# Performance work log

Hardware: AMD Instinct MI355X
Metric: run time of the kernel (lower is better)

Reference implementation:

```python
import jax, jax.numpy as jnp
import numpy as np

B, T, I, H = 256, 256, 256, 1024
STATE_DIM = 2
TAU = 0.05
MHU = 1.5


def setup_inputs() -> dict:
    key = jax.random.key(0)
    ks = jax.random.split(key, 6)
    s_in, s_h = 1.0 / np.sqrt(I), 1.0 / np.sqrt(H)
    return {
        "rnn_input": jax.random.normal(ks[0], (B, T, I), jnp.float32),
        "h0": jax.random.normal(ks[1], (1, B, H), jnp.float32),
        "c0": jax.random.normal(ks[2], (1, B, H), jnp.float32),
        "Wx": jax.random.normal(ks[3], (I, 4 * H), jnp.float32) * s_in,
        "Wh": jax.random.normal(ks[4], (H, 4 * H), jnp.float32) * s_h,
        "b": jax.random.normal(ks[5], (4 * H,), jnp.float32) * 0.01,
    }


def reference(rnn_input, h0, c0, Wx, Wh, b):
    # A: hard-coded 2x2 drift matrix applied to h[:, :STATE_DIM] for t>0
    A = jnp.array([[MHU, -MHU], [1.0 / MHU, 0.0]], dtype=rnn_input.dtype)
    hdim = Wh.shape[0]

    def step(carry, xs):
        h, c = carry                      # [B,H], [B,H]
        u_t, not_first = xs               # [B,I], scalar bool
        x_prev = h[:, :STATE_DIM]         # [B,2]
        x_next = jnp.where(not_first, x_prev + TAU * (x_prev @ A), x_prev)
        h = h.at[:, :STATE_DIM].set(x_next)
        gates = u_t @ Wx + h @ Wh + b     # [B,4H], gate order i,f,g,o
        i, f, g, o = jnp.split(gates, 4, axis=-1)
        i, f, o = jax.nn.sigmoid(i), jax.nn.sigmoid(f), jax.nn.sigmoid(o)
        g = jnp.tanh(g)
        c_next = f * c + i * g
        h_next = o * jnp.tanh(c_next)
        return (h_next, c_next), h_next

    u_seq = jnp.swapaxes(rnn_input, 0, 1)          # [T,B,I]
    not_first = jnp.arange(u_seq.shape[0]) > 0     # [T]
    (hN, cN), ys = jax.lax.scan(step, (h0[0], c0[0]), (u_seq, not_first))
    outputs = jnp.swapaxes(ys, 0, 1)               # [B,T,H] (batch_first)
    return outputs, hN[None], cN[None]
```

## Files before the change

### kernel.cpp

```cpp
#include <hip/hip_runtime.h>
#include <hip/hip_bf16.h>

#define Bdim 256
#define Tdim 256
#define Idim 256
#define Hdim 1024
#define KDIM 1280
#define NP   4096

typedef __attribute__((ext_vector_type(8)))  short short8;
typedef __attribute__((ext_vector_type(4)))  short short4v;
typedef __attribute__((ext_vector_type(16))) float f32x16;
typedef unsigned long long u64;

__device__ __forceinline__ short f2bf(float f) {
  unsigned u = __builtin_bit_cast(unsigned, f);
  unsigned r = (u + 0x7FFFu + ((u >> 16) & 1u)) >> 16;
  return (short)r;
}
__device__ __forceinline__ float bf2f(short s) {
  unsigned u = ((unsigned)(unsigned short)s) << 16;
  return __builtin_bit_cast(float, u);
}

__global__ void setup_wt_kernel(const float* __restrict__ Wx,
                                const float* __restrict__ Wh,
                                short* __restrict__ Wt) {
  __shared__ float tile[64 * 65];
  const int nb = blockIdx.x, kb = blockIdx.y;
  const int tid = threadIdx.x;
#pragma unroll
  for (int i = 0; i < 16; ++i) {
    int idx = i * 256 + tid;
    int kr = idx >> 6, nc = idx & 63;
    int kglob = kb * 64 + kr;
    int np = nb * 64 + nc;
    int col = ((np & 3) << 10) | (np >> 2);
    float v = (kglob < Idim) ? Wx[(size_t)kglob * NP + col]
                             : Wh[(size_t)(kglob - Idim) * NP + col];
    tile[kr * 65 + nc] = v;
  }
  __syncthreads();
#pragma unroll
  for (int i = 0; i < 16; ++i) {
    int idx = i * 256 + tid;
    int nr = idx >> 6, kc = idx & 63;
    Wt[(size_t)(nb * 64 + nr) * KDIM + kb * 64 + kc] = f2bf(tile[kc * 65 + nr]);
  }
}

__global__ void setup_state_kernel(const float* __restrict__ h0,
                                   const float* __restrict__ c0,
                                   const float* __restrict__ b,
                                   short* __restrict__ Uh0,
                                   float* __restrict__ c_state,
                                   float* __restrict__ bp,
                                   unsigned* __restrict__ bar) {
  if (blockIdx.x == 1041) {
    if (threadIdx.x < 256) bar[threadIdx.x] = 0u;
    return;
  }
  int idx = blockIdx.x * 256 + threadIdx.x;
  if (blockIdx.x < 1024) {
    Uh0[idx] = f2bf(h0[idx]);
    c_state[idx] = c0[idx];
  } else if (blockIdx.x < 1040) {
    int j = idx - 1024 * 256;
    if (j < NP) bp[j] = b[((j & 3) << 10) | (j >> 2)];
  }
}

__global__ __launch_bounds__(512) __attribute__((amdgpu_waves_per_eu(2, 2)))
void lstm_persistent(
    const float* __restrict__ xin,
    const short* __restrict__ Wt,
    const float* __restrict__ bp,
    short* __restrict__ Uh0,
    short* __restrict__ Uh1,
    float* __restrict__ out,
    float* __restrict__ c_state,
    float* __restrict__ hN,
    unsigned* __restrict__ bar) {
  __shared__ __align__(16) short As[32 * KDIM];
  __shared__ __align__(16) float Gred[2][32][132];

  const int tid  = threadIdx.x;
  const int lane = tid & 63;
  const int wave = tid >> 6;
  const int ntl  = wave & 3;
  const int kh   = wave >> 2;
  const int m    = blockIdx.x & 7;
  const int ng   = blockIdx.x >> 3;
  const int bm0  = m * 32;
  const int n0   = ng * 128 + ntl * 32;

  short8 Wreg[40];
  {
    const short* wr = Wt + (size_t)(n0 + (lane & 31)) * KDIM + kh * 640 + ((lane >> 5) << 3);
#pragma unroll
    for (int ks = 0; ks < 40; ++ks) Wreg[ks] = *(const short8*)(wr + ks * 16);
  }
#pragma unroll
  for (int ks = 0; ks < 40; ++ks) asm volatile("" : "+v"(Wreg[ks]));

  const int arow  = lane & 31;
  const int rbase = arow * 2560 + kh * 1280 + ((lane >> 5) << 4);
  const int rxor  = (arow & 15) << 4;

  const int row0 = tid >> 7;
  const int c8   = (tid & 127) << 3;

  const int erow = tid >> 4;
  const int ep   = tid & 15;
  const float4 bb0 = ((const float4*)bp)[ng * 32 + 2 * ep];
  const float4 bb1 = ((const float4*)bp)[ng * 32 + 2 * ep + 1];

  unsigned* flags = bar + m * 32;

  for (int t = 0; t < Tdim; ++t) {
    const short* UhR = (t & 1) ? Uh1 : Uh0;
    short* UhW = (t & 1) ? Uh0 : Uh1;

#pragma unroll
    for (int i = 0; i < 2; ++i) {
      int unit = i * 512 + tid;
      int row = unit >> 5, cx = (unit & 31) << 3;
      const float* p = xin + (size_t)(bm0 + row) * (Tdim * Idim) + (size_t)t * Idim + cx;
      float4 a = *(const float4*)p, b4 = *(const float4*)(p + 4);
      short8 v;
      v[0] = f2bf(a.x);  v[1] = f2bf(a.y);  v[2] = f2bf(a.z);  v[3] = f2bf(a.w);
      v[4] = f2bf(b4.x); v[5] = f2bf(b4.y); v[6] = f2bf(b4.z); v[7] = f2bf(b4.w);
      *(short8*)((char*)As + (((row * 2560) + (cx << 1)) ^ ((row & 15) << 4))) = v;
    }
    {
      const short* hbase = UhR + (size_t)(bm0 + row0) * Hdim + c8;
#pragma unroll
      for (int i = 0; i < 8; ++i) {
        const short* hp = hbase + (size_t)(4 * i) * Hdim;
        u64 lo = __hip_atomic_load((const u64*)hp, __ATOMIC_RELAXED,
                                   __HIP_MEMORY_SCOPE_AGENT);
        u64 hi = __hip_atomic_load((const u64*)(hp + 4), __ATOMIC_RELAXED,
                                   __HIP_MEMORY_SCOPE_AGENT);
        short4v vlo = __builtin_bit_cast(short4v, lo);
        short4v vhi = __builtin_bit_cast(short4v, hi);
        if (t > 0 && c8 == 0) {
          float x0 = bf2f(vlo[0]), x1 = bf2f(vlo[1]);
          vlo[0] = f2bf(x0 + 0.05f * (1.5f * x0 + (1.0f / 1.5f) * x1));
          vlo[1] = f2bf(x1 - 0.05f * 1.5f * x0);
        }
        int row = row0 + 4 * i;
        char* dst = (char*)As + (((row * 2560) + ((256 + c8) << 1)) ^ ((row & 15) << 4));
        *(short4v*)dst = vlo;
        *(short4v*)(dst + 8) = vhi;
      }
    }
    __syncthreads();

    f32x16 acc;
#pragma unroll
    for (int i = 0; i < 16; ++i) acc[i] = 0.f;
#pragma unroll
    for (int ks = 0; ks < 40; ++ks) {
      short8 a = *(const short8*)((char*)As + ((rbase + ks * 32) ^ rxor));
      acc = __builtin_amdgcn_mfma_f32_32x32x16_bf16(a, Wreg[ks], acc, 0, 0, 0);
    }

    {
      const int col = lane & 31, half = lane >> 5;
#pragma unroll
      for (int r = 0; r < 16; ++r) {
        int rl = (r & 3) + 8 * (r >> 2) + 4 * half;
        Gred[kh][rl][ntl * 32 + col] = acc[r];
      }
    }
    __syncthreads();

    {
      float4 a0 = *(const float4*)&Gred[0][erow][8 * ep];
      float4 a1 = *(const float4*)&Gred[0][erow][8 * ep + 4];
      float4 d0 = *(const float4*)&Gred[1][erow][8 * ep];
      float4 d1 = *(const float4*)&Gred[1][erow][8 * ep + 4];
      float gx0 = a0.x + d0.x + bb0.x, gy0 = a0.y + d0.y + bb0.y;
      float gz0 = a0.z + d0.z + bb0.z, gw0 = a0.w + d0.w + bb0.w;
      float gx1 = a1.x + d1.x + bb1.x, gy1 = a1.y + d1.y + bb1.y;
      float gz1 = a1.z + d1.z + bb1.z, gw1 = a1.w + d1.w + bb1.w;
      float iv0 = 1.0f / (1.0f + __expf(-gx0));
      float fv0 = 1.0f / (1.0f + __expf(-gy0));
      float gg0 = 2.0f / (1.0f + __expf(-2.0f * gz0)) - 1.0f;
      float ov0 = 1.0f / (1.0f + __expf(-gw0));
      float iv1 = 1.0f / (1.0f + __expf(-gx1));
      float fv1 = 1.0f / (1.0f + __expf(-gy1));
      float gg1 = 2.0f / (1.0f + __expf(-2.0f * gz1)) - 1.0f;
      float ov1 = 1.0f / (1.0f + __expf(-gw1));
      int bm = bm0 + erow;
      int hu0 = ng * 32 + 2 * ep;
      size_t cidx = (size_t)bm * Hdim + hu0;
      float2 cold = *(const float2*)&c_state[cidx];
      float cn0 = fv0 * cold.x + iv0 * gg0;
      float cn1 = fv1 * cold.y + iv1 * gg1;
      *(float2*)&c_state[cidx] = make_float2(cn0, cn1);
      float hv0 = ov0 * (2.0f / (1.0f + __expf(-2.0f * cn0)) - 1.0f);
      float hv1 = ov1 * (2.0f / (1.0f + __expf(-2.0f * cn1)) - 1.0f);
      *(float2*)&out[(size_t)bm * (Tdim * Hdim) + (size_t)t * Hdim + hu0] =
          make_float2(hv0, hv1);
      unsigned hpk = (unsigned)(unsigned short)f2bf(hv0) |
                     ((unsigned)(unsigned short)f2bf(hv1) << 16);
      __hip_atomic_store((unsigned*)&UhW[cidx], hpk, __ATOMIC_RELAXED,
                         __HIP_MEMORY_SCOPE_AGENT);
      if (t == Tdim - 1) *(float2*)&hN[cidx] = make_float2(hv0, hv1);
    }

    if (t < Tdim - 1) {
      asm volatile("s_waitcnt vmcnt(0)" ::: "memory");
      __syncthreads();
      if (wave == 0) {
        if (lane == 0)
          __hip_atomic_store(&flags[ng], (unsigned)(t + 1), __ATOMIC_RELAXED,
                             __HIP_MEMORY_SCOPE_AGENT);
        const unsigned tgt = (unsigned)(t + 1);
        for (;;) {
          unsigned v = __hip_atomic_load(&flags[lane & 31], __ATOMIC_RELAXED,
                                         __HIP_MEMORY_SCOPE_AGENT);
          if (__all((int)(v >= tgt))) break;
          __builtin_amdgcn_s_sleep(2);
        }
      }
      __syncthreads();
    }
  }
}

extern "C" void kernel_launch(void* const* d_in, const int* in_sizes, int n_in,
                              void* d_out, int out_size, void* d_ws, size_t ws_size,
                              hipStream_t stream) {
  const float* xin = (const float*)d_in[0];
  const float* h0  = (const float*)d_in[1];
  const float* c0  = (const float*)d_in[2];
  const float* Wx  = (const float*)d_in[3];
  const float* Wh  = (const float*)d_in[4];
  const float* b   = (const float*)d_in[5];
  float* out = (float*)d_out;

  char* ws = (char*)d_ws;
  short* Wt  = (short*)ws;
  short* Uh0 = (short*)(ws + 10485760);
  short* Uh1 = (short*)(ws + 10485760 + 524288);
  float* bp  = (float*)(ws + 10485760 + 1048576);
  unsigned* bar = (unsigned*)(ws + 10485760 + 1048576 + 16384);

  float* hN      = out + (size_t)Bdim * Tdim * Hdim;
  float* c_state = hN + (size_t)Bdim * Hdim;

  setup_wt_kernel<<<dim3(64, 20), 256, 0, stream>>>(Wx, Wh, Wt);
  setup_state_kernel<<<1042, 256, 0, stream>>>(h0, c0, b, Uh0, c_state, bp, bar);

  void* args[] = {(void*)&xin, (void*)&Wt, (void*)&bp, (void*)&Uh0, (void*)&Uh1,
                  (void*)&out, (void*)&c_state, (void*)&hN, (void*)&bar};
  hipLaunchCooperativeKernel((const void*)lstm_persistent, dim3(256), dim3(512),
                             args, 0, stream);
}
```

Before: 2.220 ms.

## Precompute next-step input projection during barrier wait and keep cell state in registers

Splits the shared A tile into separate input and hidden buffers. The input-projection MFMAs for step t+1 now run before the inter-block barrier wait, taking them off the critical path that follows the barrier. Input rows are prefetched two steps ahead into registers, and the cell state stays in registers, written back only once at the end. The spin-wait sleep is also shortened. The cost is more register pressure (extra prefetch registers alongside 40 weight fragments) and a changed K-split mapping of weights per wave.

```diff
diff --git a/kernel.cpp b/kernel.cpp
--- a/kernel.cpp
+++ b/kernel.cpp
@@ -81,7 +81,8 @@
     float* __restrict__ c_state,
     float* __restrict__ hN,
     unsigned* __restrict__ bar) {
-  __shared__ __align__(16) short As[32 * KDIM];
+  __shared__ __align__(16) short Asx[32 * 256];
+  __shared__ __align__(16) short Ash[32 * 1024];
   __shared__ __align__(16) float Gred[2][32][132];
 
   const int tid  = threadIdx.x;
@@ -93,19 +94,29 @@
   const int ng   = blockIdx.x >> 3;
   const int bm0  = m * 32;
   const int n0   = ng * 128 + ntl * 32;
+  const int lrow = lane & 31;
+  const int koff = (lane >> 5) << 3;
 
   short8 Wreg[40];
   {
-    const short* wr = Wt + (size_t)(n0 + (lane & 31)) * KDIM + kh * 640 + ((lane >> 5) << 3);
-#pragma unroll
-    for (int ks = 0; ks < 40; ++ks) Wreg[ks] = *(const short8*)(wr + ks * 16);
+    const short* wr = Wt + (size_t)(n0 + lrow) * KDIM + koff;
+#pragma unroll
+    for (int j = 0; j < 8; ++j)  Wreg[j]     = *(const short8*)(wr + kh * 128 + j * 16);
+#pragma unroll
+    for (int j = 0; j < 32; ++j) Wreg[8 + j] = *(const short8*)(wr + 256 + kh * 512 + j * 16);
   }
 #pragma unroll
   for (int ks = 0; ks < 40; ++ks) asm volatile("" : "+v"(Wreg[ks]));
 
-  const int arow  = lane & 31;
-  const int rbase = arow * 2560 + kh * 1280 + ((lane >> 5) << 4);
-  const int rxor  = (arow & 15) << 4;
+  const int axor = (lrow & 15) << 4;
+  const int xfb  = lrow * 512  + kh * 256  + ((lane >> 5) << 4);
+  const int hfb  = lrow * 2048 + kh * 1024 + ((lane >> 5) << 4);
+
+  const int xr = tid >> 4;
+  const int xc = (tid & 15) << 4;
+  const float* xp_base = xin + (size_t)(bm0 + xr) * (Tdim * Idim) + xc;
+  const int xw0 = xr * 512 + xc * 2;
+  const int xwx = (xr & 15) << 4;
 
   const int row0 = tid >> 7;
   const int c8   = (tid & 127) << 3;
@@ -114,29 +125,66 @@
   const int ep   = tid & 15;
   const float4 bb0 = ((const float4*)bp)[ng * 32 + 2 * ep];
   const float4 bb1 = ((const float4*)bp)[ng * 32 + 2 * ep + 1];
+  const int hu0 = ng * 32 + 2 * ep;
+  const size_t cidx = (size_t)(bm0 + erow) * Hdim + hu0;
+  float2 cReg = *(const float2*)&c_state[cidx];
+  float2 hLast = make_float2(0.f, 0.f);
 
   unsigned* flags = bar + m * 32;
+
+  {
+    const float* p = xp_base;
+    float4 a0 = *(const float4*)p,     a1 = *(const float4*)(p + 4);
+    float4 a2 = *(const float4*)(p + 8), a3 = *(const float4*)(p + 12);
+    short8 v0, v1;
+    v0[0]=f2bf(a0.x); v0[1]=f2bf(a0.y); v0[2]=f2bf(a0.z); v0[3]=f2bf(a0.w);
+    v0[4]=f2bf(a1.x); v0[5]=f2bf(a1.y); v0[6]=f2bf(a1.z); v0[7]=f2bf(a1.w);
+    v1[0]=f2bf(a2.x); v1[1]=f2bf(a2.y); v1[2]=f2bf(a2.z); v1[3]=f2bf(a2.w);
+    v1[4]=f2bf(a3.x); v1[5]=f2bf(a3.y); v1[6]=f2bf(a3.z); v1[7]=f2bf(a3.w);
+    *(short8*)((char*)Asx + (xw0 ^ xwx)) = v0;
+    *(short8*)((char*)Asx + ((xw0 + 16) ^ xwx)) = v1;
+  }
+  float4 rX0, rX1, rX2, rX3;
+  {
+    const float* p = xp_base + Idim;
+    rX0 = *(const float4*)p;      rX1 = *(const float4*)(p + 4);
+    rX2 = *(const float4*)(p + 8); rX3 = *(const float4*)(p + 12);
+  }
+  __syncthreads();
+  f32x16 acc;
+#pragma unroll
+  for (int i = 0; i < 16; ++i) acc[i] = 0.f;
+#pragma unroll
+  for (int ks = 0; ks < 8; ++ks) {
+    short8 a = *(const short8*)((char*)Asx + ((xfb + ks * 32) ^ axor));
+    acc = __builtin_amdgcn_mfma_f32_32x32x16_bf16(a, Wreg[ks], acc, 0, 0, 0);
+  }
+  __syncthreads();
 
   for (int t = 0; t < Tdim; ++t) {
     const short* UhR = (t & 1) ? Uh1 : Uh0;
     short* UhW = (t & 1) ? Uh0 : Uh1;
 
-#pragma unroll
-    for (int i = 0; i < 2; ++i) {
-      int unit = i * 512 + tid;
-      int row = unit >> 5, cx = (unit & 31) << 3;
-      const float* p = xin + (size_t)(bm0 + row) * (Tdim * Idim) + (size_t)t * Idim + cx;
-      float4 a = *(const float4*)p, b4 = *(const float4*)(p + 4);
-      short8 v;
-      v[0] = f2bf(a.x);  v[1] = f2bf(a.y);  v[2] = f2bf(a.z);  v[3] = f2bf(a.w);
-      v[4] = f2bf(b4.x); v[5] = f2bf(b4.y); v[6] = f2bf(b4.z); v[7] = f2bf(b4.w);
-      *(short8*)((char*)As + (((row * 2560) + (cx << 1)) ^ ((row & 15) << 4))) = v;
-    }
+    if (t < Tdim - 1) {
+      short8 v0, v1;
+      v0[0]=f2bf(rX0.x); v0[1]=f2bf(rX0.y); v0[2]=f2bf(rX0.z); v0[3]=f2bf(rX0.w);
+      v0[4]=f2bf(rX1.x); v0[5]=f2bf(rX1.y); v0[6]=f2bf(rX1.z); v0[7]=f2bf(rX1.w);
+      v1[0]=f2bf(rX2.x); v1[1]=f2bf(rX2.y); v1[2]=f2bf(rX2.z); v1[3]=f2bf(rX2.w);
+      v1[4]=f2bf(rX3.x); v1[5]=f2bf(rX3.y); v1[6]=f2bf(rX3.z); v1[7]=f2bf(rX3.w);
+      *(short8*)((char*)Asx + (xw0 ^ xwx)) = v0;
+      *(short8*)((char*)Asx + ((xw0 + 16) ^ xwx)) = v1;
+    }
+    if (t < Tdim - 2) {
+      const float* p = xp_base + (size_t)(t + 2) * Idim;
+      rX0 = *(const float4*)p;       rX1 = *(const float4*)(p + 4);
+      rX2 = *(const float4*)(p + 8); rX3 = *(const float4*)(p + 12);
+    }
+
     {
-      const short* hbase = UhR + (size_t)(bm0 + row0) * Hdim + c8;
+      const short* hb = UhR + (size_t)(bm0 + row0) * Hdim + c8;
 #pragma unroll
       for (int i = 0; i < 8; ++i) {
-        const short* hp = hbase + (size_t)(4 * i) * Hdim;
+        const short* hp = hb + (size_t)(4 * i) * Hdim;
         u64 lo = __hip_atomic_load((const u64*)hp, __ATOMIC_RELAXED,
                                    __HIP_MEMORY_SCOPE_AGENT);
         u64 hi = __hip_atomic_load((const u64*)(hp + 4), __ATOMIC_RELAXED,
@@ -149,20 +197,17 @@
           vlo[1] = f2bf(x1 - 0.05f * 1.5f * x0);
         }
         int row = row0 + 4 * i;
-        char* dst = (char*)As + (((row * 2560) + ((256 + c8) << 1)) ^ ((row & 15) << 4));
+        char* dst = (char*)Ash + (((row * 2048) + (c8 << 1)) ^ ((row & 15) << 4));
         *(short4v*)dst = vlo;
         *(short4v*)(dst + 8) = vhi;
       }
     }
     __syncthreads();
 
-    f32x16 acc;
-#pragma unroll
-    for (int i = 0; i < 16; ++i) acc[i] = 0.f;
-#pragma unroll
-    for (int ks = 0; ks < 40; ++ks) {
-      short8 a = *(const short8*)((char*)As + ((rbase + ks * 32) ^ rxor));
-      acc = __builtin_amdgcn_mfma_f32_32x32x16_bf16(a, Wreg[ks], acc, 0, 0, 0);
+#pragma unroll
+    for (int ks = 0; ks < 32; ++ks) {
+      short8 a = *(const short8*)((char*)Ash + ((hfb + ks * 32) ^ axor));
+      acc = __builtin_amdgcn_mfma_f32_32x32x16_bf16(a, Wreg[8 + ks], acc, 0, 0, 0);
     }
 
     {
@@ -192,25 +237,28 @@
       float fv1 = 1.0f / (1.0f + __expf(-gy1));
       float gg1 = 2.0f / (1.0f + __expf(-2.0f * gz1)) - 1.0f;
       float ov1 = 1.0f / (1.0f + __expf(-gw1));
-      int bm = bm0 + erow;
-      int hu0 = ng * 32 + 2 * ep;
-      size_t cidx = (size_t)bm * Hdim + hu0;
-      float2 cold = *(const float2*)&c_state[cidx];
-      float cn0 = fv0 * cold.x + iv0 * gg0;
-      float cn1 = fv1 * cold.y + iv1 * gg1;
-      *(float2*)&c_state[cidx] = make_float2(cn0, cn1);
+      float cn0 = fv0 * cReg.x + iv0 * gg0;
+      float cn1 = fv1 * cReg.y + iv1 * gg1;
+      cReg = make_float2(cn0, cn1);
       float hv0 = ov0 * (2.0f / (1.0f + __expf(-2.0f * cn0)) - 1.0f);
       float hv1 = ov1 * (2.0f / (1.0f + __expf(-2.0f * cn1)) - 1.0f);
-      *(float2*)&out[(size_t)bm * (Tdim * Hdim) + (size_t)t * Hdim + hu0] =
-          make_float2(hv0, hv1);
       unsigned hpk = (unsigned)(unsigned short)f2bf(hv0) |
                      ((unsigned)(unsigned short)f2bf(hv1) << 16);
       __hip_atomic_store((unsigned*)&UhW[cidx], hpk, __ATOMIC_RELAXED,
                          __HIP_MEMORY_SCOPE_AGENT);
-      if (t == Tdim - 1) *(float2*)&hN[cidx] = make_float2(hv0, hv1);
+      *(float2*)&out[(size_t)(bm0 + erow) * (Tdim * Hdim) + (size_t)t * Hdim + hu0] =
+          make_float2(hv0, hv1);
+      hLast = make_float2(hv0, hv1);
     }
 
     if (t < Tdim - 1) {
+#pragma unroll
+      for (int i = 0; i < 16; ++i) acc[i] = 0.f;
+#pragma unroll
+      for (int ks = 0; ks < 8; ++ks) {
+        short8 a = *(const short8*)((char*)Asx + ((xfb + ks * 32) ^ axor));
+        acc = __builtin_amdgcn_mfma_f32_32x32x16_bf16(a, Wreg[ks], acc, 0, 0, 0);
+      }
       asm volatile("s_waitcnt vmcnt(0)" ::: "memory");
       __syncthreads();
       if (wave == 0) {
@@ -222,12 +270,15 @@
           unsigned v = __hip_atomic_load(&flags[lane & 31], __ATOMIC_RELAXED,
                                          __HIP_MEMORY_SCOPE_AGENT);
           if (__all((int)(v >= tgt))) break;
-          __builtin_amdgcn_s_sleep(2);
+          __builtin_amdgcn_s_sleep(1);
         }
       }
       __syncthreads();
     }
   }
+
+  *(float2*)&c_state[cidx] = cReg;
+  *(float2*)&hN[cidx] = hLast;
 }
 
 extern "C" void kernel_launch(void* const* d_in, const int* in_sizes, int n_in,
```

New measurement: 2.336 ms. 1.05x slower.
